# Kernel optimization log

Hardware: AMD Instinct MI355X
Metric: run time of the kernel (lower is better)

## Reference

```python
import jax, jax.numpy as jnp
import numpy as np

SCALING_FACTOR = 1.0


def setup_inputs() -> dict:
    key = jax.random.key(0)
    k1, k2, k3 = jax.random.split(key, 3)
    B, N1, N2, DX, DZ, NT, NK = 4, 64, 64, 2, 128, 2048, 2
    x_grid = jax.random.uniform(k1, (B, N1, N2, DX), dtype=jnp.float32)
    z_grid = jax.random.normal(k2, (B, N1, N2, DZ), dtype=jnp.float32)
    xt = jax.random.uniform(k3, (B, NT, DX), dtype=jnp.float32)
    # Replicates torch init: logspace around log10(init_lengthscale), inverse-softplus
    init_ls = np.logspace(np.log10(0.1) - 0.5, np.log10(0.1) + 0.5, NK).astype(np.float32)
    init_ls = np.tile(init_ls[None, :], (DX, 1))  # (dim, num_kernels)
    lengthscale_param = jnp.asarray(np.log(np.expm1(init_ls)))
    return {"x_grid": x_grid, "z_grid": z_grid, "xt": xt, "lengthscale_param": lengthscale_param}


def reference(x_grid, z_grid, xt, lengthscale_param):
    B = x_grid.shape[0]
    xg = x_grid.reshape(B, -1, x_grid.shape[-1])   # (b, ng, dx)
    zg = z_grid.reshape(B, -1, z_grid.shape[-1])   # (b, ng, dz)
    ls = 1e-5 + jax.nn.softplus(lengthscale_param)  # (dx, nk)
    # EQ/RBF weights: (b, nt, ng, nk)
    diff = (xt[:, :, None, :, None] - xg[:, None, :, :, None]) / ls[None, None, None]
    weights = jnp.exp(-0.5 * jnp.sum(diff * diff, axis=3))
    # weighted smoothing: per-kernel matmul weights @ z_grid, then interleave as (dz nk)
    out = jnp.einsum('btgk,bgz->btzk', weights, zg) / SCALING_FACTOR  # (b, nt, dz, nk)
    return out.reshape(B, xt.shape[1], -1)  # (b, nt, dz*nk), nk fastest like 'b nt (dz nk)'
```

## Files before the change

kernel.cpp:

```cpp
#include <hip/hip_runtime.h>
#include <hip/hip_bf16.h>
#include <cmath>

#define B_   4
#define NT_  2048
#define G_   4096
#define DZ_  128

typedef __attribute__((ext_vector_type(8))) short bf16x8;
typedef __attribute__((ext_vector_type(4))) float f32x4;

__device__ __forceinline__ float softplus_f(float x) {
    return fmaxf(x, 0.0f) + log1pf(expf(-fabsf(x)));
}

__device__ __forceinline__ void gl2lds16(const void* gsrc, void* ldst) {
    __builtin_amdgcn_global_load_lds(
        (const __attribute__((address_space(1))) unsigned int*)gsrc,
        (__attribute__((address_space(3))) unsigned int*)ldst, 16, 0, 0);
}

__global__ __launch_bounds__(256, 1)
void transpose_z(const float* __restrict__ z, unsigned short* __restrict__ zt)
{
    __shared__ unsigned short tile[64][66];
    const int bx = blockIdx.x;
    const int zti = bx & 1;
    const int gt  = (bx >> 1) & 63;
    const int b   = bx >> 7;
    const int g0 = gt * 64, z0 = zti * 64;
    const int tid = threadIdx.x;
    const int zl = tid & 63, gl = tid >> 6;
    #pragma unroll
    for (int i = 0; i < 16; ++i) {
        const int g = gl + i * 4;
        const float v = z[(size_t)(b * G_ + g0 + g) * DZ_ + z0 + zl];
        unsigned int u = __float_as_uint(v);
        u = u + 0x7FFFu + ((u >> 16) & 1u);
        tile[g][zl] = (unsigned short)(u >> 16);
    }
    __syncthreads();
    const int gp = (tid & 31) * 2, zi = tid >> 5;
    const int c  = (g0 + gp) >> 5, gi = gp & 31;
    #pragma unroll
    for (int i = 0; i < 8; ++i) {
        const int zz = zi + i * 8;
        const unsigned int lo = tile[gp][zz], hi = tile[gp + 1][zz];
        *(unsigned int*)(zt + ((size_t)(b * 128 + c) * 128 + z0 + zz) * 32 + gi)
            = lo | (hi << 16);
    }
}

__global__ __launch_bounds__(512, 4)
void setconv_main(const float* __restrict__ xt,
                  const float* __restrict__ xg,
                  const float* __restrict__ lsp,
                  const unsigned short* __restrict__ Zt,
                  float* __restrict__ out)
{
    __shared__ __align__(16) unsigned short lds[32768];

    const int bx = blockIdx.x;
    const int b  = (bx >> 1) & 3;
    const int tt = ((bx >> 3) << 1) | (bx & 1);
    const int tid  = threadIdx.x;
    const int w    = tid >> 6;
    const int lane = tid & 63;
    const int quad = lane >> 4;
    const int l15  = lane & 15;
    const int t0   = tt * 16;

    float c00, c01, c10, c11;
    {
        const float h = -0.72134752f;
        float ls;
        ls = 1e-5f + softplus_f(lsp[0]); c00 = h / (ls * ls);
        ls = 1e-5f + softplus_f(lsp[1]); c01 = h / (ls * ls);
        ls = 1e-5f + softplus_f(lsp[2]); c10 = h / (ls * ls);
        ls = 1e-5f + softplus_f(lsp[3]); c11 = h / (ls * ls);
    }

    const float xt0 = xt[(size_t)(b * NT_ + t0 + l15) * 2 + 0];
    const float xt1 = xt[(size_t)(b * NT_ + t0 + l15) * 2 + 1];

    f32x4 acc[2][8];
    #pragma unroll
    for (int k = 0; k < 2; ++k)
        #pragma unroll
        for (int n = 0; n < 8; ++n) acc[k][n] = (f32x4)0.0f;

    unsigned short* const mytile = lds + w * 4096;
    const float* xgq = xg + (size_t)(b * G_ + w * 512 + quad * 8) * 2;

    float4 xv0 = *(const float4*)(xgq + 0);
    float4 xv1 = *(const float4*)(xgq + 4);
    float4 xv2 = *(const float4*)(xgq + 8);
    float4 xv3 = *(const float4*)(xgq + 12);
    {
        const unsigned short* zs = Zt + (size_t)(b * 128 + w * 16) * 4096 + lane * 8;
        #pragma unroll
        for (int i = 0; i < 8; ++i)
            gl2lds16(zs + i * 512, mytile + i * 512);
    }

    #pragma unroll
    for (int ch = 0; ch < 16; ++ch) {
        float gx[8], gy[8];
        gx[0]=xv0.x; gy[0]=xv0.y; gx[1]=xv0.z; gy[1]=xv0.w;
        gx[2]=xv1.x; gy[2]=xv1.y; gx[3]=xv1.z; gy[3]=xv1.w;
        gx[4]=xv2.x; gy[4]=xv2.y; gx[5]=xv2.z; gy[5]=xv2.w;
        gx[6]=xv3.x; gy[6]=xv3.y; gx[7]=xv3.z; gy[7]=xv3.w;
        unsigned int w0b[8], w1b[8];
        #pragma unroll
        for (int j = 0; j < 8; ++j) {
            const float d0 = xt0 - gx[j];
            const float d1 = xt1 - gy[j];
            const float q0 = d0 * d0;
            const float q1 = d1 * d1;
            const float e0 = fmaf(q1, c10, q0 * c00);
            const float e1 = fmaf(q1, c11, q0 * c01);
            w0b[j] = __float_as_uint(__builtin_amdgcn_exp2f(e0));
            w1b[j] = __float_as_uint(__builtin_amdgcn_exp2f(e1));
        }
        union { bf16x8 v; unsigned int u[4]; } a0, a1;
        #pragma unroll
        for (int h = 0; h < 4; ++h) {
            a0.u[h] = __builtin_amdgcn_perm(w0b[2*h+1], w0b[2*h], 0x07060302u);
            a1.u[h] = __builtin_amdgcn_perm(w1b[2*h+1], w1b[2*h], 0x07060302u);
        }

        __builtin_amdgcn_s_waitcnt(0x0F70);
        if (ch < 15) {
            const float* xp = xgq + (ch + 1) * 64;
            xv0 = *(const float4*)(xp + 0);
            xv1 = *(const float4*)(xp + 4);
            xv2 = *(const float4*)(xp + 8);
            xv3 = *(const float4*)(xp + 12);
        }

        #pragma unroll
        for (int nt = 0; nt < 8; ++nt) {
            const bf16x8 bz = *(const bf16x8*)(mytile + nt * 512 + l15 * 32 + quad * 8);
            acc[0][nt] = __builtin_amdgcn_mfma_f32_16x16x32_bf16(a0.v, bz, acc[0][nt], 0, 0, 0);
            acc[1][nt] = __builtin_amdgcn_mfma_f32_16x16x32_bf16(a1.v, bz, acc[1][nt], 0, 0, 0);
        }

        if (ch < 15) {
            const unsigned short* zs = Zt + (size_t)(b * 128 + w * 16 + ch + 1) * 4096
                                       + lane * 8;
            #pragma unroll
            for (int i = 0; i < 8; ++i)
                gl2lds16(zs + i * 512, mytile + i * 512);
        }
    }

    float* const red = (float*)lds;
    #define RED_W(slot) { \
        float* bp = &red[(slot) * 4096 + lane * 4]; \
        _Pragma("unroll") \
        for (int k = 0; k < 2; ++k) \
            _Pragma("unroll") \
            for (int n = 0; n < 8; ++n) \
                *(f32x4*)(bp + (k * 8 + n) * 256) = acc[k][n]; }
    #define RED_A(slot) { \
        const float* bp = &red[(slot) * 4096 + lane * 4]; \
        _Pragma("unroll") \
        for (int k = 0; k < 2; ++k) \
            _Pragma("unroll") \
            for (int n = 0; n < 8; ++n) \
                acc[k][n] += *(const f32x4*)(bp + (k * 8 + n) * 256); }

    __syncthreads();
    if (w >= 4) RED_W(w - 4);
    __syncthreads();
    if (w < 4) RED_A(w);
    if (w == 2 || w == 3) RED_W(w);
    __syncthreads();
    if (w < 2) RED_A(w + 2);
    if (w == 1) RED_W(3);
    __syncthreads();
    if (w == 0) {
        RED_A(3);
        const int tr = t0 + quad * 4;
        #pragma unroll
        for (int nt = 0; nt < 8; ++nt) {
            float* ob = out + (size_t)(b * NT_ + tr) * (DZ_ * 2) + (nt * 16 + l15) * 2;
            #pragma unroll
            for (int r = 0; r < 4; ++r)
                *(float2*)(ob + (size_t)r * (DZ_ * 2)) =
                    make_float2(acc[0][nt][r], acc[1][nt][r]);
        }
    }
    #undef RED_W
    #undef RED_A
}

extern "C" void kernel_launch(void* const* d_in, const int* in_sizes, int n_in,
                              void* d_out, int out_size, void* d_ws, size_t ws_size,
                              hipStream_t stream)
{
    const float* x_grid = (const float*)d_in[0];
    const float* z_grid = (const float*)d_in[1];
    const float* xt     = (const float*)d_in[2];
    const float* lsp    = (const float*)d_in[3];
    float* out = (float*)d_out;
    unsigned short* Zt = (unsigned short*)d_ws;

    hipLaunchKernelGGL(transpose_z, dim3(512), dim3(256), 0, stream, z_grid, Zt);
    hipLaunchKernelGGL(setconv_main, dim3(512), dim3(512), 0, stream,
                       xt, x_grid, lsp, Zt, out);
}
```

Before: 103.2 us.

## Process 32 targets per block with double-buffered LDS Z tiles

Each block now covers two 16-target subtiles, so every Z tile read from LDS feeds twice as many MFMAs. The grid halves to 256 blocks and the Z global-to-LDS staging is double buffered, prefetching two chunks ahead. The cost is twice the accumulators per wave and twice the LDS per block, with launch bounds relaxed from 4 to 2 blocks. That lowers occupancy, and 256 blocks may leave the device underfilled.

```diff
diff --git a/kernel.cpp b/kernel.cpp
--- a/kernel.cpp
+++ b/kernel.cpp
@@ -51,24 +51,24 @@
     }
 }
 
-__global__ __launch_bounds__(512, 4)
+__global__ __launch_bounds__(512, 2)
 void setconv_main(const float* __restrict__ xt,
                   const float* __restrict__ xg,
                   const float* __restrict__ lsp,
                   const unsigned short* __restrict__ Zt,
                   float* __restrict__ out)
 {
-    __shared__ __align__(16) unsigned short lds[32768];
+    __shared__ __align__(16) unsigned short lds[65536];
 
     const int bx = blockIdx.x;
-    const int b  = (bx >> 1) & 3;
-    const int tt = ((bx >> 3) << 1) | (bx & 1);
+    const int b  = bx & 3;
+    const int tt = bx >> 2;
     const int tid  = threadIdx.x;
     const int w    = tid >> 6;
     const int lane = tid & 63;
     const int quad = lane >> 4;
     const int l15  = lane & 15;
-    const int t0   = tt * 16;
+    const int t0   = tt * 32;
 
     float c00, c01, c10, c11;
     {
@@ -80,28 +80,34 @@
         ls = 1e-5f + softplus_f(lsp[3]); c11 = h / (ls * ls);
     }
 
-    const float xt0 = xt[(size_t)(b * NT_ + t0 + l15) * 2 + 0];
-    const float xt1 = xt[(size_t)(b * NT_ + t0 + l15) * 2 + 1];
-
-    f32x4 acc[2][8];
-    #pragma unroll
-    for (int k = 0; k < 2; ++k)
+    const float xtA0 = xt[(size_t)(b * NT_ + t0 + l15) * 2 + 0];
+    const float xtA1 = xt[(size_t)(b * NT_ + t0 + l15) * 2 + 1];
+    const float xtB0 = xt[(size_t)(b * NT_ + t0 + 16 + l15) * 2 + 0];
+    const float xtB1 = xt[(size_t)(b * NT_ + t0 + 16 + l15) * 2 + 1];
+
+    f32x4 acc[2][2][8];
+    #pragma unroll
+    for (int ts = 0; ts < 2; ++ts)
         #pragma unroll
-        for (int n = 0; n < 8; ++n) acc[k][n] = (f32x4)0.0f;
-
-    unsigned short* const mytile = lds + w * 4096;
+        for (int k = 0; k < 2; ++k)
+            #pragma unroll
+            for (int n = 0; n < 8; ++n) acc[ts][k][n] = (f32x4)0.0f;
+
+    unsigned short* const buf0 = lds + w * 8192;
+    unsigned short* const buf1 = buf0 + 4096;
     const float* xgq = xg + (size_t)(b * G_ + w * 512 + quad * 8) * 2;
+    const unsigned short* zs = Zt + (size_t)(b * 128 + w * 16) * 4096 + lane * 8;
 
     float4 xv0 = *(const float4*)(xgq + 0);
     float4 xv1 = *(const float4*)(xgq + 4);
     float4 xv2 = *(const float4*)(xgq + 8);
     float4 xv3 = *(const float4*)(xgq + 12);
-    {
-        const unsigned short* zs = Zt + (size_t)(b * 128 + w * 16) * 4096 + lane * 8;
-        #pragma unroll
-        for (int i = 0; i < 8; ++i)
-            gl2lds16(zs + i * 512, mytile + i * 512);
-    }
+    #pragma unroll
+    for (int i = 0; i < 8; ++i)
+        gl2lds16(zs + i * 512, buf0 + i * 512);
+    #pragma unroll
+    for (int i = 0; i < 8; ++i)
+        gl2lds16(zs + 4096 + i * 512, buf1 + i * 512);
 
     #pragma unroll
     for (int ch = 0; ch < 16; ++ch) {
@@ -110,26 +116,48 @@
         gx[2]=xv1.x; gy[2]=xv1.y; gx[3]=xv1.z; gy[3]=xv1.w;
         gx[4]=xv2.x; gy[4]=xv2.y; gx[5]=xv2.z; gy[5]=xv2.w;
         gx[6]=xv3.x; gy[6]=xv3.y; gx[7]=xv3.z; gy[7]=xv3.w;
-        unsigned int w0b[8], w1b[8];
-        #pragma unroll
-        for (int j = 0; j < 8; ++j) {
-            const float d0 = xt0 - gx[j];
-            const float d1 = xt1 - gy[j];
-            const float q0 = d0 * d0;
-            const float q1 = d1 * d1;
-            const float e0 = fmaf(q1, c10, q0 * c00);
-            const float e1 = fmaf(q1, c11, q0 * c01);
-            w0b[j] = __float_as_uint(__builtin_amdgcn_exp2f(e0));
-            w1b[j] = __float_as_uint(__builtin_amdgcn_exp2f(e1));
-        }
-        union { bf16x8 v; unsigned int u[4]; } a0, a1;
-        #pragma unroll
-        for (int h = 0; h < 4; ++h) {
-            a0.u[h] = __builtin_amdgcn_perm(w0b[2*h+1], w0b[2*h], 0x07060302u);
-            a1.u[h] = __builtin_amdgcn_perm(w1b[2*h+1], w1b[2*h], 0x07060302u);
-        }
-
-        __builtin_amdgcn_s_waitcnt(0x0F70);
+        union { bf16x8 v; unsigned int u[4]; } aA0, aA1, aB0, aB1;
+        {
+            unsigned int w0b[8], w1b[8];
+            #pragma unroll
+            for (int j = 0; j < 8; ++j) {
+                const float d0 = xtA0 - gx[j];
+                const float d1 = xtA1 - gy[j];
+                const float q0 = d0 * d0;
+                const float q1 = d1 * d1;
+                const float e0 = fmaf(q1, c10, q0 * c00);
+                const float e1 = fmaf(q1, c11, q0 * c01);
+                w0b[j] = __float_as_uint(__builtin_amdgcn_exp2f(e0));
+                w1b[j] = __float_as_uint(__builtin_amdgcn_exp2f(e1));
+            }
+            #pragma unroll
+            for (int h = 0; h < 4; ++h) {
+                aA0.u[h] = __builtin_amdgcn_perm(w0b[2*h+1], w0b[2*h], 0x07060302u);
+                aA1.u[h] = __builtin_amdgcn_perm(w1b[2*h+1], w1b[2*h], 0x07060302u);
+            }
+        }
+        {
+            unsigned int w0b[8], w1b[8];
+            #pragma unroll
+            for (int j = 0; j < 8; ++j) {
+                const float d0 = xtB0 - gx[j];
+                const float d1 = xtB1 - gy[j];
+                const float q0 = d0 * d0;
+                const float q1 = d1 * d1;
+                const float e0 = fmaf(q1, c10, q0 * c00);
+                const float e1 = fmaf(q1, c11, q0 * c01);
+                w0b[j] = __float_as_uint(__builtin_amdgcn_exp2f(e0));
+                w1b[j] = __float_as_uint(__builtin_amdgcn_exp2f(e1));
+            }
+            #pragma unroll
+            for (int h = 0; h < 4; ++h) {
+                aB0.u[h] = __builtin_amdgcn_perm(w0b[2*h+1], w0b[2*h], 0x07060302u);
+                aB1.u[h] = __builtin_amdgcn_perm(w1b[2*h+1], w1b[2*h], 0x07060302u);
+            }
+        }
+
+        __builtin_amdgcn_s_waitcnt(0x0F78);
+
         if (ch < 15) {
             const float* xp = xgq + (ch + 1) * 64;
             xv0 = *(const float4*)(xp + 0);
@@ -138,37 +166,58 @@
             xv3 = *(const float4*)(xp + 12);
         }
 
+        const unsigned short* tile = (ch & 1) ? buf1 : buf0;
         #pragma unroll
         for (int nt = 0; nt < 8; ++nt) {
-            const bf16x8 bz = *(const bf16x8*)(mytile + nt * 512 + l15 * 32 + quad * 8);
-            acc[0][nt] = __builtin_amdgcn_mfma_f32_16x16x32_bf16(a0.v, bz, acc[0][nt], 0, 0, 0);
-            acc[1][nt] = __builtin_amdgcn_mfma_f32_16x16x32_bf16(a1.v, bz, acc[1][nt], 0, 0, 0);
-        }
-
-        if (ch < 15) {
-            const unsigned short* zs = Zt + (size_t)(b * 128 + w * 16 + ch + 1) * 4096
-                                       + lane * 8;
+            const bf16x8 bz = *(const bf16x8*)(tile + nt * 512 + l15 * 32 + quad * 8);
+            acc[0][0][nt] = __builtin_amdgcn_mfma_f32_16x16x32_bf16(aA0.v, bz, acc[0][0][nt], 0, 0, 0);
+            acc[0][1][nt] = __builtin_amdgcn_mfma_f32_16x16x32_bf16(aA1.v, bz, acc[0][1][nt], 0, 0, 0);
+            acc[1][0][nt] = __builtin_amdgcn_mfma_f32_16x16x32_bf16(aB0.v, bz, acc[1][0][nt], 0, 0, 0);
+            acc[1][1][nt] = __builtin_amdgcn_mfma_f32_16x16x32_bf16(aB1.v, bz, acc[1][1][nt], 0, 0, 0);
+        }
+
+        if (ch < 14) {
+            const unsigned short* zc = zs + (size_t)(ch + 2) * 4096;
+            unsigned short* dst = (ch & 1) ? buf1 : buf0;
             #pragma unroll
             for (int i = 0; i < 8; ++i)
-                gl2lds16(zs + i * 512, mytile + i * 512);
+                gl2lds16(zc + i * 512, dst + i * 512);
         }
     }
 
     float* const red = (float*)lds;
     #define RED_W(slot) { \
-        float* bp = &red[(slot) * 4096 + lane * 4]; \
+        float* bp = &red[(slot) * 8192 + lane * 4]; \
+        _Pragma("unroll") \
+        for (int ts = 0; ts < 2; ++ts) \
+            _Pragma("unroll") \
+            for (int k = 0; k < 2; ++k) \
+                _Pragma("unroll") \
+                for (int n = 0; n < 8; ++n) \
+                    *(f32x4*)(bp + (ts * 16 + k * 8 + n) * 256) = acc[ts][k][n]; }
+    #define RED_A(slot) { \
+        const float* bp = &red[(slot) * 8192 + lane * 4]; \
+        _Pragma("unroll") \
+        for (int ts = 0; ts < 2; ++ts) \
+            _Pragma("unroll") \
+            for (int k = 0; k < 2; ++k) \
+                _Pragma("unroll") \
+                for (int n = 0; n < 8; ++n) \
+                    acc[ts][k][n] += *(const f32x4*)(bp + (ts * 16 + k * 8 + n) * 256); }
+    #define RED_W_T(slot, ts) { \
+        float* bp = &red[(slot) * 8192 + lane * 4]; \
         _Pragma("unroll") \
         for (int k = 0; k < 2; ++k) \
             _Pragma("unroll") \
             for (int n = 0; n < 8; ++n) \
-                *(f32x4*)(bp + (k * 8 + n) * 256) = acc[k][n]; }
-    #define RED_A(slot) { \
-        const float* bp = &red[(slot) * 4096 + lane * 4]; \
+                *(f32x4*)(bp + (k * 8 + n) * 256) = acc[ts][k][n]; }
+    #define RED_A_T(slot, ts) { \
+        const float* bp = &red[(slot) * 8192 + lane * 4]; \
         _Pragma("unroll") \
         for (int k = 0; k < 2; ++k) \
             _Pragma("unroll") \
             for (int n = 0; n < 8; ++n) \
-                acc[k][n] += *(const f32x4*)(bp + (k * 8 + n) * 256); }
+                acc[ts][k][n] += *(const f32x4*)(bp + (k * 8 + n) * 256); }
 
     __syncthreads();
     if (w >= 4) RED_W(w - 4);
@@ -177,22 +226,26 @@
     if (w == 2 || w == 3) RED_W(w);
     __syncthreads();
     if (w < 2) RED_A(w + 2);
-    if (w == 1) RED_W(3);
-    __syncthreads();
-    if (w == 0) {
-        RED_A(3);
-        const int tr = t0 + quad * 4;
+    if (w == 1) RED_W_T(3, 0);
+    if (w == 0) RED_W_T(2, 1);
+    __syncthreads();
+    if (w < 2) {
+        if (w == 0) { RED_A_T(3, 0); } else { RED_A_T(2, 1); }
+        const int ts = w;
+        const int tr = t0 + ts * 16 + quad * 4;
         #pragma unroll
         for (int nt = 0; nt < 8; ++nt) {
             float* ob = out + (size_t)(b * NT_ + tr) * (DZ_ * 2) + (nt * 16 + l15) * 2;
             #pragma unroll
             for (int r = 0; r < 4; ++r)
                 *(float2*)(ob + (size_t)r * (DZ_ * 2)) =
-                    make_float2(acc[0][nt][r], acc[1][nt][r]);
+                    make_float2(acc[ts][0][nt][r], acc[ts][1][nt][r]);
         }
     }
     #undef RED_W
     #undef RED_A
+    #undef RED_W_T
+    #undef RED_A_T
 }
 
 extern "C" void kernel_launch(void* const* d_in, const int* in_sizes, int n_in,
@@ -207,6 +260,6 @@
     unsigned short* Zt = (unsigned short*)d_ws;
 
     hipLaunchKernelGGL(transpose_z, dim3(512), dim3(256), 0, stream, z_grid, Zt);
-    hipLaunchKernelGGL(setconv_main, dim3(512), dim3(512), 0, stream,
+    hipLaunchKernelGGL(setconv_main, dim3(256), dim3(512), 0, stream,
                        xt, x_grid, lsp, Zt, out);
 }
```

Result: slower. 220.7 us (+113.8%).
